# Kernel tuning notes

Measured on AMD Instinct MI355X. Metric: run time of the kernel, lower is better.

Reference implementation:

```python
import jax, jax.numpy as jnp
import numpy as np
import math

NUM_PAGES = 256   # total KV pool pages
PAGE_SIZE = 16    # tokens per page
N_USED = 128      # pages in this sequence -> kv_len = 2048
H = 32            # num_heads
D = 128           # head_dim
LQ = 2048         # query length (== kv_len, causal prefill)


def setup_inputs() -> dict:
    key = jax.random.key(0)
    k_q, k_k, k_v, k_ks, k_vs = jax.random.split(key, 5)
    q = jax.random.normal(k_q, (1, H, LQ, D), dtype=jnp.float32)
    K_pages = jax.random.randint(k_k, (NUM_PAGES, PAGE_SIZE, H, D), -128, 128, dtype=jnp.int8)
    V_pages = jax.random.randint(k_v, (NUM_PAGES, PAGE_SIZE, H, D), -128, 128, dtype=jnp.int8)
    K_scale = jax.random.uniform(k_ks, (NUM_PAGES, 1, H, 1), dtype=jnp.float16, minval=0.001, maxval=0.02)
    V_scale = jax.random.uniform(k_vs, (NUM_PAGES, 1, H, 1), dtype=jnp.float16, minval=0.001, maxval=0.02)
    pages = jnp.arange(N_USED, dtype=jnp.int32)  # page table for this sequence
    return {"q": q, "K_pages": K_pages, "V_pages": V_pages,
            "K_scale": K_scale, "V_scale": V_scale, "pages": pages}


def _gather_dequant(pages_i8, scales, page_ids):
    # pages_i8: [P, ps, H, D] int8; scales: [P, 1, H, 1] fp16; page_ids: [n]
    x = pages_i8[page_ids].astype(jnp.float32) * scales[page_ids].astype(jnp.float32)
    n, ps, h, d = x.shape
    # cat along tokens, then [S,H,D] -> [1,H,S,D]
    return jnp.transpose(x.reshape(n * ps, h, d), (1, 0, 2))[None]


def reference(q, K_pages, V_pages, K_scale, V_scale, pages):
    K = _gather_dequant(K_pages, K_scale, pages)  # [1,H,S,D]
    V = _gather_dequant(V_pages, V_scale, pages)  # [1,H,S,D]
    lq = q.shape[2]
    s = K.shape[2]
    scale = 1.0 / math.sqrt(q.shape[-1])
    scores = jnp.einsum('bhqd,bhkd->bhqk', q, K) * scale  # [1,H,LQ,S]
    # torch is_causal: top-left aligned causal mask (j <= i)
    causal = jnp.tril(jnp.ones((lq, s), dtype=bool))
    scores = jnp.where(causal[None, None], scores, -jnp.inf)
    attn = jax.nn.softmax(scores, axis=-1)
    return jnp.einsum('bhqk,bhkd->bhqd', attn, V)
```

## Files before the change

### kernel.cpp

```cpp
#include <hip/hip_runtime.h>
#include <stdint.h>

#define NHEADS 32
#define DHEAD  128
#define LQ     2048
#define PAGE   16
#define QTILE  64
#define NQT    32
#define KVB    32
#define KPAD   136

typedef _Float16 f16x8 __attribute__((ext_vector_type(8)));
typedef float    f32x4 __attribute__((ext_vector_type(4)));

__global__ __launch_bounds__(256, 2)
void paged_attn_kernel(const float* __restrict__ q,
                       const int*   __restrict__ Kp,
                       const int*   __restrict__ Vp,
                       const float* __restrict__ Kscale,
                       const float* __restrict__ Vscale,
                       const int*   __restrict__ pages,
                       float* __restrict__ out)
{
    __shared__ _Float16 Ks[KVB][KPAD];
    __shared__ __align__(16) _Float16 Vt[DHEAD][KVB];
    __shared__ float    ksc[KVB];
    __shared__ _Float16 Ps[4][16][40];

    const int tid  = threadIdx.x;
    const int w    = tid >> 6;
    const int lane = tid & 63;
    const int g    = lane >> 4;
    const int c    = lane & 15;

    const int bx = blockIdx.x;
    const int h  = bx & (NHEADS - 1);
    const int p  = bx >> 5;
    const int qa = p, qb = NQT - 1 - p;
    const int q0a = qa * QTILE, q0b = qb * QTILE;

    const float qscale = 0.08838834764831845f * 1.44269504088896340736f;

    f16x8 qfa[4], qfb[4];
    {
        const float* qpa = q + ((size_t)h * LQ + q0a + w * 16 + c) * DHEAD;
        const float* qpb = q + ((size_t)h * LQ + q0b + w * 16 + c) * DHEAD;
        #pragma unroll
        for (int t = 0; t < 4; ++t) {
            #pragma unroll
            for (int i = 0; i < 8; ++i) {
                qfa[t][i] = (_Float16)(qpa[t * 32 + g * 8 + i] * qscale);
                qfb[t][i] = (_Float16)(qpb[t * 32 + g * 8 + i] * qscale);
            }
        }
    }

    f32x4 oaccA[8], oaccB[8];
    float mA[4], lA[4], mB[4], lB[4];
    #pragma unroll
    for (int d = 0; d < 8; ++d) { oaccA[d] = (f32x4){0,0,0,0}; oaccB[d] = (f32x4){0,0,0,0}; }
    #pragma unroll
    for (int r = 0; r < 4; ++r) { mA[r] = mB[r] = -1e30f; lA[r] = lB[r] = 0.f; }

    const int ntiles = 2 * qb + 2;
    const int skv = tid >> 3;
    const int sa  = tid & 7;

    char* vtb = (char*)&Vt[0][0];

    auto issue = [&](int tile, int4* krD, int4* vrD, float& ksD, float& vsD) {
        const int t_glob = tile * KVB + skv;
        const int pg  = pages[t_glob >> 4];
        const int tok = t_glob & 15;
        const size_t base = (((size_t)pg * PAGE + tok) * NHEADS + h) * DHEAD + sa * 16;
        const int4* kp4 = (const int4*)(Kp + base);
        const int4* vp4 = (const int4*)(Vp + base);
        #pragma unroll
        for (int j = 0; j < 4; ++j) { krD[j] = kp4[j]; vrD[j] = vp4[j]; }
        vsD = Vscale[pg * NHEADS + h];
        if (tid < KVB) {
            const int pg2 = pages[(tile * KVB + tid) >> 4];
            ksD = Kscale[pg2 * NHEADS + h];
        }
    };

    auto compute = [&](int kv0, const f16x8* qf, int q0t,
                       f32x4* oacc, float* mr, float* lr) {
        f32x4 s[2];
        #pragma unroll
        for (int nt = 0; nt < 2; ++nt) {
            s[nt] = (f32x4){0,0,0,0};
            #pragma unroll
            for (int t = 0; t < 4; ++t) {
                f16x8 kf = *(const f16x8*)&Ks[nt * 16 + c][t * 32 + g * 8];
                s[nt] = __builtin_amdgcn_mfma_f32_16x16x32_f16(qf[t], kf, s[nt], 0, 0, 0);
            }
        }
        const float ks0 = ksc[c],  ks1 = ksc[16 + c];
        const int kvg0 = kv0 + c, kvg1 = kv0 + 16 + c;
        const int qg   = q0t + w * 16 + g * 4;

        float tmax[4];
        #pragma unroll
        for (int r = 0; r < 4; ++r) {
            float s0 = s[0][r] * ks0;
            float s1 = s[1][r] * ks1;
            if (kvg0 > qg + r) s0 = -1e30f;
            if (kvg1 > qg + r) s1 = -1e30f;
            s[0][r] = s0; s[1][r] = s1;
            tmax[r] = fmaxf(s0, s1);
        }
        #pragma unroll
        for (int off = 1; off < 16; off <<= 1)
            #pragma unroll
            for (int r = 0; r < 4; ++r)
                tmax[r] = fmaxf(tmax[r], __shfl_xor(tmax[r], off, 64));
        float alpha[4], rsum[4], p0[4], p1[4];
        #pragma unroll
        for (int r = 0; r < 4; ++r) {
            const float mn = fmaxf(mr[r], tmax[r]);
            alpha[r] = exp2f(mr[r] - mn);
            mr[r] = mn;
            p0[r] = exp2f(s[0][r] - mn);
            p1[r] = exp2f(s[1][r] - mn);
            rsum[r] = p0[r] + p1[r];
        }
        #pragma unroll
        for (int off = 1; off < 16; off <<= 1)
            #pragma unroll
            for (int r = 0; r < 4; ++r)
                rsum[r] += __shfl_xor(rsum[r], off, 64);
        #pragma unroll
        for (int r = 0; r < 4; ++r)
            lr[r] = lr[r] * alpha[r] + rsum[r];
        #pragma unroll
        for (int d = 0; d < 8; ++d)
            #pragma unroll
            for (int r = 0; r < 4; ++r)
                oacc[d][r] *= alpha[r];

        #pragma unroll
        for (int r = 0; r < 4; ++r) {
            Ps[w][g * 4 + r][c]      = (_Float16)p0[r];
            Ps[w][g * 4 + r][16 + c] = (_Float16)p1[r];
        }
        asm volatile("s_waitcnt lgkmcnt(0)" ::: "memory");
        f16x8 pf = *(const f16x8*)&Ps[w][c][g * 8];

        #pragma unroll
        for (int d = 0; d < 8; ++d) {
            const int dcol = d * 16 + c;
            unsigned off = (unsigned)(dcol * (KVB * 2) + g * 16);
            off ^= (unsigned)(((dcol >> 3) & 7) << 4);
            f16x8 vf = *(const f16x8*)(vtb + off);
            oacc[d] = __builtin_amdgcn_mfma_f32_16x16x32_f16(pf, vf, oacc[d], 0, 0, 0);
        }
    };

    int4 krA[4], vrA[4]; float kscA = 0.f, vsrA = 0.f;
    int4 krB[4], vrB[4]; float kscB = 0.f, vsrB = 0.f;
    issue(0, krA, vrA, kscA, vsrA);

    for (int tile = 0; tile < ntiles; ++tile) {
        const int kv0 = tile * KVB;

        {
            const int* ki = (const int*)krA;
            const int* vi = (const int*)vrA;
            f16x8 klo, khi;
            #pragma unroll
            for (int i = 0; i < 8; ++i) {
                klo[i] = (_Float16)ki[i];
                khi[i] = (_Float16)ki[8 + i];
            }
            *(f16x8*)&Ks[skv][sa * 16]     = klo;
            *(f16x8*)&Ks[skv][sa * 16 + 8] = khi;
            #pragma unroll
            for (int j = 0; j < 16; ++j) {
                const int dcol = sa * 16 + j;
                unsigned off = (unsigned)(dcol * (KVB * 2) + skv * 2);
                off ^= (unsigned)(((dcol >> 3) & 7) << 4);
                *(_Float16*)(vtb + off) = (_Float16)((float)vi[j] * vsrA);
            }
            if (tid < KVB) ksc[tid] = kscA;
        }
        __syncthreads();

        if (tile + 1 < ntiles) issue(tile + 1, krB, vrB, kscB, vsrB);

        if (kv0 <= q0b + w * 16 + 15)
            compute(kv0, qfb, q0b, oaccB, mB, lB);
        if (kv0 <= q0a + w * 16 + 15)
            compute(kv0, qfa, q0a, oaccA, mA, lA);

        __syncthreads();

        if (tile + 1 < ntiles) {
            #pragma unroll
            for (int j = 0; j < 4; ++j) { krA[j] = krB[j]; vrA[j] = vrB[j]; }
            kscA = kscB; vsrA = vsrB;
        }
    }

    #pragma unroll
    for (int r = 0; r < 4; ++r) { lA[r] = 1.f / lA[r]; lB[r] = 1.f / lB[r]; }
    const int qgA = q0a + w * 16 + g * 4;
    const int qgB = q0b + w * 16 + g * 4;
    #pragma unroll
    for (int d = 0; d < 8; ++d) {
        #pragma unroll
        for (int r = 0; r < 4; ++r) {
            out[((size_t)h * LQ + qgA + r) * DHEAD + d * 16 + c] = oaccA[d][r] * lA[r];
            out[((size_t)h * LQ + qgB + r) * DHEAD + d * 16 + c] = oaccB[d][r] * lB[r];
        }
    }
}

extern "C" void kernel_launch(void* const* d_in, const int* in_sizes, int n_in,
                              void* d_out, int out_size, void* d_ws, size_t ws_size,
                              hipStream_t stream) {
    (void)in_sizes; (void)n_in; (void)d_ws; (void)ws_size; (void)out_size;
    const float* qp = (const float*)d_in[0];
    const int*   kp = (const int*)d_in[1];
    const int*   vp = (const int*)d_in[2];
    const float* ks = (const float*)d_in[3];
    const float* vs = (const float*)d_in[4];
    const int*   pg = (const int*)d_in[5];
    float*       op = (float*)d_out;

    dim3 grid(NHEADS * (NQT / 2));
    dim3 block(256);
    paged_attn_kernel<<<grid, block, 0, stream>>>(qp, kp, vp, ks, vs, pg, op);
}
```

Baseline: 315.8 us.

## Compute transposed S=K·Q^T so softmax reduces in-lane, pass P via shuffles

```diff
diff --git a/kernel.cpp b/kernel.cpp
--- a/kernel.cpp
+++ b/kernel.cpp
@@ -11,6 +11,7 @@
 #define KPAD   136
 
 typedef _Float16 f16x8 __attribute__((ext_vector_type(8)));
+typedef _Float16 f16x2v __attribute__((ext_vector_type(2)));
 typedef float    f32x4 __attribute__((ext_vector_type(4)));
 
 __global__ __launch_bounds__(256, 2)
@@ -24,8 +25,6 @@
 {
     __shared__ _Float16 Ks[KVB][KPAD];
     __shared__ __align__(16) _Float16 Vt[DHEAD][KVB];
-    __shared__ float    ksc[KVB];
-    __shared__ _Float16 Ps[4][16][40];
 
     const int tid  = threadIdx.x;
     const int w    = tid >> 6;
@@ -46,26 +45,22 @@
         const float* qpa = q + ((size_t)h * LQ + q0a + w * 16 + c) * DHEAD;
         const float* qpb = q + ((size_t)h * LQ + q0b + w * 16 + c) * DHEAD;
         #pragma unroll
-        for (int t = 0; t < 4; ++t) {
+        for (int t = 0; t < 4; ++t)
             #pragma unroll
             for (int i = 0; i < 8; ++i) {
                 qfa[t][i] = (_Float16)(qpa[t * 32 + g * 8 + i] * qscale);
                 qfb[t][i] = (_Float16)(qpb[t * 32 + g * 8 + i] * qscale);
             }
-        }
     }
 
     f32x4 oaccA[8], oaccB[8];
-    float mA[4], lA[4], mB[4], lB[4];
     #pragma unroll
     for (int d = 0; d < 8; ++d) { oaccA[d] = (f32x4){0,0,0,0}; oaccB[d] = (f32x4){0,0,0,0}; }
-    #pragma unroll
-    for (int r = 0; r < 4; ++r) { mA[r] = mB[r] = -1e30f; lA[r] = lB[r] = 0.f; }
+    float mA = -1e30f, lA = 0.f, mB = -1e30f, lB = 0.f;
 
     const int ntiles = 2 * qb + 2;
     const int skv = tid >> 3;
     const int sa  = tid & 7;
-
     char* vtb = (char*)&Vt[0][0];
 
     auto issue = [&](int tile, int4* krD, int4* vrD, float& ksD, float& vsD) {
@@ -77,89 +72,85 @@
         const int4* vp4 = (const int4*)(Vp + base);
         #pragma unroll
         for (int j = 0; j < 4; ++j) { krD[j] = kp4[j]; vrD[j] = vp4[j]; }
+        ksD = Kscale[pg * NHEADS + h];
         vsD = Vscale[pg * NHEADS + h];
-        if (tid < KVB) {
-            const int pg2 = pages[(tile * KVB + tid) >> 4];
-            ksD = Kscale[pg2 * NHEADS + h];
-        }
     };
 
-    auto compute = [&](int kv0, const f16x8* qf, int q0t,
-                       f32x4* oacc, float* mr, float* lr) {
-        f32x4 s[2];
-        #pragma unroll
-        for (int nt = 0; nt < 2; ++nt) {
-            s[nt] = (f32x4){0,0,0,0};
-            #pragma unroll
-            for (int t = 0; t < 4; ++t) {
-                f16x8 kf = *(const f16x8*)&Ks[nt * 16 + c][t * 32 + g * 8];
-                s[nt] = __builtin_amdgcn_mfma_f32_16x16x32_f16(qf[t], kf, s[nt], 0, 0, 0);
-            }
-        }
-        const float ks0 = ksc[c],  ks1 = ksc[16 + c];
-        const int kvg0 = kv0 + c, kvg1 = kv0 + 16 + c;
-        const int qg   = q0t + w * 16 + g * 4;
-
-        float tmax[4];
+    auto compute = [&](int kv0, const f16x8 (*kf)[4], const f16x8* qf, int q0t,
+                       f32x4* oacc, float& mr, float& lr) {
+        f32x4 s0 = (f32x4){0,0,0,0}, s1 = (f32x4){0,0,0,0};
+        #pragma unroll
+        for (int t = 0; t < 4; ++t) {
+            s0 = __builtin_amdgcn_mfma_f32_16x16x32_f16(kf[0][t], qf[t], s0, 0, 0, 0);
+            s1 = __builtin_amdgcn_mfma_f32_16x16x32_f16(kf[1][t], qf[t], s1, 0, 0, 0);
+        }
+        const int dq = (q0t + w * 16 + c) - (kv0 + 4 * g);
         #pragma unroll
         for (int r = 0; r < 4; ++r) {
-            float s0 = s[0][r] * ks0;
-            float s1 = s[1][r] * ks1;
-            if (kvg0 > qg + r) s0 = -1e30f;
-            if (kvg1 > qg + r) s1 = -1e30f;
-            s[0][r] = s0; s[1][r] = s1;
-            tmax[r] = fmaxf(s0, s1);
-        }
-        #pragma unroll
-        for (int off = 1; off < 16; off <<= 1)
+            if (r > dq)      s0[r] = -1e30f;
+            if (r > dq - 16) s1[r] = -1e30f;
+        }
+        float tm = fmaxf(fmaxf(fmaxf(s0[0], s0[1]), fmaxf(s0[2], s0[3])),
+                         fmaxf(fmaxf(s1[0], s1[1]), fmaxf(s1[2], s1[3])));
+        tm = fmaxf(tm, __shfl_xor(tm, 16, 64));
+        tm = fmaxf(tm, __shfl_xor(tm, 32, 64));
+        const float mn    = fmaxf(mr, tm);
+        const float alpha = exp2f(mr - mn);
+        mr = mn;
+        float p0[4], p1[4];
+        #pragma unroll
+        for (int r = 0; r < 4; ++r) {
+            p0[r] = exp2f(s0[r] - mn);
+            p1[r] = exp2f(s1[r] - mn);
+        }
+        float rs = ((p0[0] + p0[1]) + (p0[2] + p0[3])) +
+                   ((p1[0] + p1[1]) + (p1[2] + p1[3]));
+        rs += __shfl_xor(rs, 16, 64);
+        rs += __shfl_xor(rs, 32, 64);
+        lr = lr * alpha + rs;
+        float aR[4];
+        #pragma unroll
+        for (int r = 0; r < 4; ++r) aR[r] = __shfl(alpha, 20 * g + r, 64);
+        #pragma unroll
+        for (int d = 0; d < 8; ++d)
             #pragma unroll
             for (int r = 0; r < 4; ++r)
-                tmax[r] = fmaxf(tmax[r], __shfl_xor(tmax[r], off, 64));
-        float alpha[4], rsum[4], p0[4], p1[4];
-        #pragma unroll
-        for (int r = 0; r < 4; ++r) {
-            const float mn = fmaxf(mr[r], tmax[r]);
-            alpha[r] = exp2f(mr[r] - mn);
-            mr[r] = mn;
-            p0[r] = exp2f(s[0][r] - mn);
-            p1[r] = exp2f(s[1][r] - mn);
-            rsum[r] = p0[r] + p1[r];
-        }
-        #pragma unroll
-        for (int off = 1; off < 16; off <<= 1)
-            #pragma unroll
-            for (int r = 0; r < 4; ++r)
-                rsum[r] += __shfl_xor(rsum[r], off, 64);
-        #pragma unroll
-        for (int r = 0; r < 4; ++r)
-            lr[r] = lr[r] * alpha[r] + rsum[r];
-        #pragma unroll
-        for (int d = 0; d < 8; ++d)
-            #pragma unroll
-            for (int r = 0; r < 4; ++r)
-                oacc[d][r] *= alpha[r];
-
-        #pragma unroll
-        for (int r = 0; r < 4; ++r) {
-            Ps[w][g * 4 + r][c]      = (_Float16)p0[r];
-            Ps[w][g * 4 + r][16 + c] = (_Float16)p1[r];
-        }
-        asm volatile("s_waitcnt lgkmcnt(0)" ::: "memory");
-        f16x8 pf = *(const f16x8*)&Ps[w][c][g * 8];
-
+                oacc[d][r] *= aR[r];
+        f16x2v t0, t1, t2, t3;
+        t0[0] = (_Float16)p0[0]; t0[1] = (_Float16)p0[1];
+        t1[0] = (_Float16)p0[2]; t1[1] = (_Float16)p0[3];
+        t2[0] = (_Float16)p1[0]; t2[1] = (_Float16)p1[1];
+        t3[0] = (_Float16)p1[2]; t3[1] = (_Float16)p1[3];
+        const int w00 = __builtin_bit_cast(int, t0);
+        const int w01 = __builtin_bit_cast(int, t1);
+        const int w10 = __builtin_bit_cast(int, t2);
+        const int w11 = __builtin_bit_cast(int, t3);
+        const int srcL = ((g & 1) << 5) | c;
+        const int srcH = srcL + 16;
+        const int e0A = __shfl(w00, srcL, 64), e0B = __shfl(w10, srcL, 64);
+        const int e1A = __shfl(w01, srcL, 64), e1B = __shfl(w11, srcL, 64);
+        const int e2A = __shfl(w00, srcH, 64), e2B = __shfl(w10, srcH, 64);
+        const int e3A = __shfl(w01, srcH, 64), e3B = __shfl(w11, srcH, 64);
+        const bool hi = g >= 2;
+        uint4 aw;
+        aw.x = (unsigned)(hi ? e0B : e0A);
+        aw.y = (unsigned)(hi ? e1B : e1A);
+        aw.z = (unsigned)(hi ? e2B : e2A);
+        aw.w = (unsigned)(hi ? e3B : e3A);
+        const f16x8 pa = __builtin_bit_cast(f16x8, aw);
         #pragma unroll
         for (int d = 0; d < 8; ++d) {
             const int dcol = d * 16 + c;
             unsigned off = (unsigned)(dcol * (KVB * 2) + g * 16);
             off ^= (unsigned)(((dcol >> 3) & 7) << 4);
             f16x8 vf = *(const f16x8*)(vtb + off);
-            oacc[d] = __builtin_amdgcn_mfma_f32_16x16x32_f16(pf, vf, oacc[d], 0, 0, 0);
+            oacc[d] = __builtin_amdgcn_mfma_f32_16x16x32_f16(pa, vf, oacc[d], 0, 0, 0);
         }
     };
 
-    int4 krA[4], vrA[4]; float kscA = 0.f, vsrA = 0.f;
-    int4 krB[4], vrB[4]; float kscB = 0.f, vsrB = 0.f;
-    issue(0, krA, vrA, kscA, vsrA);
+    int4 krA[4], vrA[4]; float ksrA = 0.f, vsrA = 0.f;
+    int4 krB[4], vrB[4]; float ksrB = 0.f, vsrB = 0.f;
+    issue(0, krA, vrA, ksrA, vsrA);
 
     for (int tile = 0; tile < ntiles; ++tile) {
         const int kv0 = tile * KVB;
@@ -170,8 +161,8 @@
             f16x8 klo, khi;
             #pragma unroll
             for (int i = 0; i < 8; ++i) {
-                klo[i] = (_Float16)ki[i];
-                khi[i] = (_Float16)ki[8 + i];
+                klo[i] = (_Float16)((float)ki[i]     * ksrA);
+                khi[i] = (_Float16)((float)ki[8 + i] * ksrA);
             }
             *(f16x8*)&Ks[skv][sa * 16]     = klo;
             *(f16x8*)&Ks[skv][sa * 16 + 8] = khi;
@@ -182,38 +173,47 @@
                 off ^= (unsigned)(((dcol >> 3) & 7) << 4);
                 *(_Float16*)(vtb + off) = (_Float16)((float)vi[j] * vsrA);
             }
-            if (tid < KVB) ksc[tid] = kscA;
         }
         __syncthreads();
 
-        if (tile + 1 < ntiles) issue(tile + 1, krB, vrB, kscB, vsrB);
+        if (tile + 1 < ntiles) issue(tile + 1, krB, vrB, ksrB, vsrB);
+
+        f16x8 kf[2][4];
+        #pragma unroll
+        for (int t = 0; t < 4; ++t) {
+            kf[0][t] = *(const f16x8*)&Ks[c][t * 32 + g * 8];
+            kf[1][t] = *(const f16x8*)&Ks[16 + c][t * 32 + g * 8];
+        }
 
         if (kv0 <= q0b + w * 16 + 15)
-            compute(kv0, qfb, q0b, oaccB, mB, lB);
+            compute(kv0, kf, qfb, q0b, oaccB, mB, lB);
         if (kv0 <= q0a + w * 16 + 15)
-            compute(kv0, qfa, q0a, oaccA, mA, lA);
+            compute(kv0, kf, qfa, q0a, oaccA, mA, lA);
 
         __syncthreads();
 
         if (tile + 1 < ntiles) {
             #pragma unroll
             for (int j = 0; j < 4; ++j) { krA[j] = krB[j]; vrA[j] = vrB[j]; }
-            kscA = kscB; vsrA = vsrB;
+            ksrA = ksrB; vsrA = vsrB;
         }
     }
 
+    float iA[4], iB[4];
     #pragma unroll
-    for (int r = 0; r < 4; ++r) { lA[r] = 1.f / lA[r]; lB[r] = 1.f / lB[r]; }
+    for (int r = 0; r < 4; ++r) {
+        iA[r] = 1.f / __shfl(lA, 20 * g + r, 64);
+        iB[r] = 1.f / __shfl(lB, 20 * g + r, 64);
+    }
     const int qgA = q0a + w * 16 + g * 4;
     const int qgB = q0b + w * 16 + g * 4;
     #pragma unroll
-    for (int d = 0; d < 8; ++d) {
+    for (int d = 0; d < 8; ++d)
         #pragma unroll
         for (int r = 0; r < 4; ++r) {
-            out[((size_t)h * LQ + qgA + r) * DHEAD + d * 16 + c] = oaccA[d][r] * lA[r];
-            out[((size_t)h * LQ + qgB + r) * DHEAD + d * 16 + c] = oaccB[d][r] * lB[r];
-        }
-    }
+            out[((size_t)h * LQ + qgA + r) * DHEAD + d * 16 + c] = oaccA[d][r] * iA[r];
+            out[((size_t)h * LQ + qgB + r) * DHEAD + d * 16 + c] = oaccB[d][r] * iB[r];
+        }
 }
 
 extern "C" void kernel_launch(void* const* d_in, const int* in_sizes, int n_in,
```

After: 265.3 us. 16.0% less time.
